# Kernel optimization log

Hardware: AMD Instinct MI355X
Metric: run time of the kernel (lower is better)

Reference implementation:

```python
import jax, jax.numpy as jnp
import numpy as np

B, S, D, H = 128, 256, 256, 8   # graphs, nodes/graph, dim_h, heads
N = B * S
E = 524288
DH = D // H
BN_EPS = 1e-5

def _bn(v, g, b):
    # BatchNorm1d forward with batch statistics (biased var), eval-dropout model
    m = v.mean(0)
    var = v.var(0)
    return (v - m) * jax.lax.rsqrt(var + BN_EPS) * g + b

def setup_inputs() -> dict:
    key = jax.random.key(0)
    ks = jax.random.split(key, 40)
    x = jax.random.normal(ks[0], (N, D), jnp.float32)
    src = jax.random.randint(ks[1], (E,), 0, N)
    dst = (src // S) * S + jax.random.randint(ks[2], (E,), 0, S)  # intra-graph edges
    edge_index = jnp.stack([src, dst]).astype(jnp.int64)
    def lin(k, i, o):
        return (jax.random.normal(k, (i, o), jnp.float32) / np.float32(np.sqrt(i)))
    inp = {
        'x': x, 'edge_index': edge_index,
        'W_gcn': lin(ks[3], D, D), 'b_gcn': jnp.zeros((D,), jnp.float32),
        'W_gin1': lin(ks[4], D, D), 'b_gin1': jnp.zeros((D,), jnp.float32),
        'W_gin2': lin(ks[5], D, D), 'b_gin2': jnp.zeros((D,), jnp.float32),
        'g_kv': jnp.ones((D,), jnp.float32), 'be_kv': jnp.zeros((D,), jnp.float32),
        'Wq1': lin(ks[6], D, D), 'bq1': jnp.zeros((D,), jnp.float32),
        'Wq2': lin(ks[7], D, D), 'bq2': jnp.zeros((D,), jnp.float32),
        'Wq_a': lin(ks[8], D, D), 'bq_a': jnp.zeros((D,), jnp.float32),
        'Wk_a': lin(ks[9], D, D), 'bk_a': jnp.zeros((D,), jnp.float32),
        'Wv_a': lin(ks[10], D, D), 'bv_a': jnp.zeros((D,), jnp.float32),
        'Wo_a': lin(ks[11], D, D), 'bo_a': jnp.zeros((D,), jnp.float32),
        'g_attn': jnp.ones((D,), jnp.float32), 'be_attn': jnp.zeros((D,), jnp.float32),
        'Wf1': lin(ks[12], D, 2 * D), 'bf1': jnp.zeros((2 * D,), jnp.float32),
        'Wf2': lin(ks[13], 2 * D, D), 'bf2': jnp.zeros((D,), jnp.float32),
        'g2': jnp.ones((D,), jnp.float32), 'be2': jnp.zeros((D,), jnp.float32),
    }
    return inp

def _forward(x, edge_index,
             W_gcn, b_gcn, W_gin1, b_gin1, W_gin2, b_gin2, g_kv, be_kv,
             Wq1, bq1, Wq2, bq2,
             Wq_a, bq_a, Wk_a, bk_a, Wv_a, bv_a, Wo_a, bo_a, g_attn, be_attn,
             Wf1, bf1, Wf2, bf2, g2, be2):
    row, col = edge_index[0], edge_index[1]
    h_in1 = x

    # ---- expert 0: GCNConv (add self loops + symmetric norm) ----
    loops = jnp.arange(N, dtype=row.dtype)
    row2 = jnp.concatenate([row, loops])
    col2 = jnp.concatenate([col, loops])
    deg = jax.ops.segment_sum(jnp.ones_like(row2, jnp.float32), col2, num_segments=N)
    dinv = jnp.where(deg > 0, jax.lax.rsqrt(deg), 0.0)
    norm = dinv[row2] * dinv[col2]                     # [E+N]
    xw = x @ W_gcn                                      # [N, D]
    h_gcn = jax.ops.segment_sum(norm[:, None] * xw[row2], col2, num_segments=N) + b_gcn
    e0 = _bn(h_gcn, g_kv, be_kv)

    # ---- expert 1: GINConv (eps=0, sum aggregation, 2-layer MLP) ----
    agg = jax.ops.segment_sum(x[row], col, num_segments=N)
    h_gin = jax.nn.relu((x + agg) @ W_gin1 + b_gin1) @ W_gin2 + b_gin2
    e1 = _bn(h_gin, g_kv, be_kv)

    # ---- global expert normalization (torch .std -> unbiased) ----
    allo = jnp.concatenate([e0, e1], axis=0)
    gm = allo.mean()
    gs = jnp.std(allo, ddof=1)
    e0 = (e0 - gm) / (gs + 1e-8)
    e1 = (e1 - gm) / (gs + 1e-8)

    # ---- uniform routing & kv residual mix ----
    kv = 0.5 * e0 + 0.5 * e1 + 0.1 * h_in1              # [N, D]

    # ---- dense batching (equal-sized graphs -> pure reshape, full mask) ----
    q_dense = h_in1.reshape(B, S, D)
    kv_dense = kv.reshape(B, S, D)

    # ---- q projection MLP ----
    q_dense = jax.nn.relu(q_dense @ Wq1 + bq1) @ Wq2 + bq2

    # ---- multihead attention (batch_first, no padding) ----
    qh = (q_dense @ Wq_a + bq_a).reshape(B, S, H, DH)
    kh = (kv_dense @ Wk_a + bk_a).reshape(B, S, H, DH)
    vh = (kv_dense @ Wv_a + bv_a).reshape(B, S, H, DH)
    scores = jnp.einsum('bqhd,bkhd->bhqk', qh, kh) / np.float32(np.sqrt(DH))
    attn = jax.nn.softmax(scores, axis=-1)
    o = jnp.einsum('bhqk,bkhd->bqhd', attn, vh).reshape(B, S, D)
    h_attn = (o @ Wo_a + bo_a).reshape(N, D)

    # ---- residual + norm + FFN block ----
    h = _bn(h_in1 + h_attn, g_attn, be_attn)
    h_ff = jax.nn.relu(h @ Wf1 + bf1) @ Wf2 + bf2
    h = _bn(h + h_ff, g2, be2)
    return h

def reference(x, edge_index,
              W_gcn, b_gcn, W_gin1, b_gin1, W_gin2, b_gin2, g_kv, be_kv,
              Wq1, bq1, Wq2, bq2,
              Wq_a, bq_a, Wk_a, bk_a, Wv_a, bv_a, Wo_a, bo_a, g_attn, be_attn,
              Wf1, bf1, Wf2, bf2, g2, be2):
    return _forward(x, edge_index,
                    W_gcn, b_gcn, W_gin1, b_gin1, W_gin2, b_gin2, g_kv, be_kv,
                    Wq1, bq1, Wq2, bq2,
                    Wq_a, bq_a, Wk_a, bk_a, Wv_a, bv_a, Wo_a, bo_a, g_attn, be_attn,
                    Wf1, bf1, Wf2, bf2, g2, be2)
```

## Files before the change

### kernel.cpp

```cpp
#include <hip/hip_runtime.h>
#include <hip/hip_bf16.h>

typedef __hip_bfloat16 bf16;
typedef __attribute__((ext_vector_type(8))) short short8;
typedef __attribute__((ext_vector_type(4))) short short4v;
typedef __attribute__((ext_vector_type(4))) float f32x4;
typedef __attribute__((ext_vector_type(4))) int i32x4;

#define N_ 32768
#define D_ 256
#define S_ 256
#define B_ 128
#define E_ 524288

static __device__ __forceinline__ f32x4 mfma16(short8 a, short8 b, f32x4 c) {
  return __builtin_amdgcn_mfma_f32_16x16x32_bf16(a, b, c, 0, 0, 0);
}
static __device__ __forceinline__ f32x4 fzero4() {
  f32x4 z; z[0] = 0.f; z[1] = 0.f; z[2] = 0.f; z[3] = 0.f; return z;
}
static __device__ __forceinline__ float bits2f(short s) {
  unsigned u = ((unsigned)(unsigned short)s) << 16;
  return __builtin_bit_cast(float, u);
}
static __device__ __forceinline__ short f2bits(float f) {
  bf16 b = __float2bfloat16(f);
  return __builtin_bit_cast(short, b);
}

#define GLOAD_LDS16(G, L) __builtin_amdgcn_global_load_lds( \
    (const __attribute__((address_space(1))) void*)(G),     \
    (__attribute__((address_space(3))) void*)(L), 16, 0, 0)

template<int F>
__global__ __launch_bounds__(256)
void gemm_bt(const bf16* __restrict__ A, const bf16* __restrict__ Bt,
             const float* __restrict__ bias, const float* __restrict__ biasB,
             const void* __restrict__ resid,
             float* __restrict__ Cf, bf16* __restrict__ Cb,
             float* __restrict__ Sp, float* __restrict__ SSp,
             int M, int Nc, int K, long bsA, long bsB, long bsC)
{
  __shared__ __align__(16) bf16 lA[128 * 32];
  __shared__ __align__(16) bf16 lB[128 * 32];
  __shared__ float sS[2][128], sSS[2][128];
  const int z = blockIdx.z;
  const bf16* Ab = A + (long)z * bsA;
  const bf16* Bb = Bt + (long)z * bsB;
  const int m0 = blockIdx.x * 128, n0 = blockIdx.y * 128;
  const int tid = threadIdx.x;
  const int lane = tid & 63;
  const int w = tid >> 6, wr = w >> 1, wc = w & 1;
  const int g = lane >> 4, r = lane & 15, ko = g * 8;
  const int srow = lane >> 2, skw = (lane & 3) * 8;

  f32x4 acc[4][4];
  for (int i = 0; i < 4; i++) for (int j = 0; j < 4; j++) acc[i][j] = fzero4();

  for (int k0 = 0; k0 < K; k0 += 32) {
    __syncthreads();
    for (int i = 0; i < 2; i++) {
      const int c = w * 2 + i;
      GLOAD_LDS16(Ab + (long)(m0 + c * 16 + srow) * K + k0 + skw, lA + c * 512);
      GLOAD_LDS16(Bb + (long)(n0 + c * 16 + srow) * K + k0 + skw, lB + c * 512);
    }
    __syncthreads();
    short8 af[4], bfv[4];
    for (int mi = 0; mi < 4; mi++)
      af[mi] = *(const short8*)&lA[(wr * 64 + mi * 16 + r) * 32 + ko];
    for (int ni = 0; ni < 4; ni++)
      bfv[ni] = *(const short8*)&lB[(wc * 64 + ni * 16 + r) * 32 + ko];
    for (int mi = 0; mi < 4; mi++)
      for (int ni = 0; ni < 4; ni++)
        acc[mi][ni] = mfma16(af[mi], bfv[ni], acc[mi][ni]);
  }

  float cs[4] = {0, 0, 0, 0}, css[4] = {0, 0, 0, 0};
  for (int mi = 0; mi < 4; mi++) for (int ni = 0; ni < 4; ni++) {
    const int row = m0 + wr * 64 + mi * 16 + g * 4;
    const int col = n0 + wc * 64 + ni * 16 + r;
    float bv = 0.0f;
    if (F & 2) {
      if ((F & 128) && col >= 256) bv = biasB[col - 256];
      else bv = bias[col];
    }
    for (int j = 0; j < 4; j++) {
      long idx = (long)(row + j) * Nc + col;
      float v = acc[mi][ni][j] + bv;
      if (F & 4)  v += ((const float*)resid)[(long)z * bsC + idx];
      if (F & 64) v += bits2f(((const short*)resid)[(long)z * bsC + idx]);
      if (F & 1)  v = fmaxf(v, 0.0f);
      if (F & 32) { cs[ni] += v; css[ni] += v * v; }
      if (F & 8)  Cf[(long)z * bsC + idx] = v;
      if (F & 16) Cb[(long)z * bsC + idx] = __float2bfloat16(v);
    }
  }
  if (F & 32) {
    for (int ni = 0; ni < 4; ni++) {
      cs[ni]  += __shfl_xor(cs[ni], 16);  cs[ni]  += __shfl_xor(cs[ni], 32);
      css[ni] += __shfl_xor(css[ni], 16); css[ni] += __shfl_xor(css[ni], 32);
    }
    if (lane < 16) {
      for (int ni = 0; ni < 4; ni++) {
        sS[wr][wc * 64 + ni * 16 + lane]  = cs[ni];
        sSS[wr][wc * 64 + ni * 16 + lane] = css[ni];
      }
    }
    __syncthreads();
    if (tid < 128) {
      atomicAdd(&Sp[n0 + tid],  sS[0][tid] + sS[1][tid]);
      atomicAdd(&SSp[n0 + tid], sSS[0][tid] + sSS[1][tid]);
    }
  }
}

template<int NS, int EP1, int EP2, bool STATS>
static __device__ __forceinline__ void mlp_body(
    const bf16* __restrict__ A, const bf16* __restrict__ B1,
    const bf16* __restrict__ B2, const bf16* __restrict__ B3,
    const float* __restrict__ bEp1, const float* __restrict__ bEp2,
    const float* __restrict__ bFin, const bf16* __restrict__ resid,
    bf16* __restrict__ out, float* __restrict__ Sp, float* __restrict__ SSp,
    bf16* lA, bf16* lB, bf16* lC)
{
  char* lCc = (char*)lC;
  const int tid = threadIdx.x;
  const int lane = tid & 63;
  const int w = tid >> 6;
  const int mh = w >> 2, nq = w & 3;
  const int g = lane >> 4, r = lane & 15, ko = g * 8;

  f32x4 acc[2][4];
  for (int i = 0; i < 2; i++) for (int j = 0; j < 4; j++) acc[i][j] = fzero4();

  for (int k0 = 0; k0 < 256; k0 += 32) {
    __syncthreads();
    if (tid < 256)
      GLOAD_LDS16(A + (long)(tid >> 2) * 256 + k0 + (tid & 3) * 8, lA + w * 512);
    GLOAD_LDS16(B1 + (long)(tid >> 2) * 256 + k0 + (tid & 3) * 8, lB + w * 512);
    GLOAD_LDS16(B1 + (long)((tid + 512) >> 2) * 256 + k0 + ((tid + 512) & 3) * 8,
                lB + w * 512 + 4096);
    __syncthreads();
    short8 af[2], bfv[4];
    for (int mi = 0; mi < 2; mi++)
      af[mi] = *(const short8*)&lA[(mh * 32 + mi * 16 + r) * 32 + ko];
    for (int ni = 0; ni < 4; ni++)
      bfv[ni] = *(const short8*)&lB[(nq * 64 + ni * 16 + r) * 32 + ko];
    for (int mi = 0; mi < 2; mi++)
      for (int ni = 0; ni < 4; ni++)
        acc[mi][ni] = mfma16(af[mi], bfv[ni], acc[mi][ni]);
  }
  for (int mi = 0; mi < 2; mi++) for (int ni = 0; ni < 4; ni++) {
    const int col = nq * 64 + ni * 16 + r;
    const float bv = (EP1 & 1) ? bEp1[col] : 0.0f;
    for (int j = 0; j < 4; j++) {
      const int row = mh * 32 + mi * 16 + g * 4 + j;
      float v = acc[mi][ni][j] + bv;
      if (EP1 & 4) v += bits2f(__builtin_bit_cast(short, resid[(long)row * 256 + col]));
      if (EP1 & 2) v = fmaxf(v, 0.0f);
      *(short*)(lCc + ((row * 512 + col * 2) ^ ((row & 7) << 4))) = f2bits(v);
    }
  }
  __syncthreads();

  for (int s = 2; s <= NS; s++) {
    const bf16* Bs = (s == 2) ? B2 : B3;
    for (int i = 0; i < 2; i++) for (int j = 0; j < 4; j++) acc[i][j] = fzero4();
    for (int k0 = 0; k0 < 256; k0 += 32) {
      __syncthreads();
      GLOAD_LDS16(Bs + (long)(tid >> 2) * 256 + k0 + (tid & 3) * 8, lB + w * 512);
      GLOAD_LDS16(Bs + (long)((tid + 512) >> 2) * 256 + k0 + ((tid + 512) & 3) * 8,
                  lB + w * 512 + 4096);
      __syncthreads();
      short8 af[2], bfv[4];
      for (int mi = 0; mi < 2; mi++) {
        const int row = mh * 32 + mi * 16 + r;
        af[mi] = *(const short8*)(lCc +
                  ((row * 512 + (k0 + ko) * 2) ^ ((row & 7) << 4)));
      }
      for (int ni = 0; ni < 4; ni++)
        bfv[ni] = *(const short8*)&lB[(nq * 64 + ni * 16 + r) * 32 + ko];
      for (int mi = 0; mi < 2; mi++)
        for (int ni = 0; ni < 4; ni++)
          acc[mi][ni] = mfma16(af[mi], bfv[ni], acc[mi][ni]);
    }
    if (s < NS) {
      __syncthreads();
      for (int mi = 0; mi < 2; mi++) for (int ni = 0; ni < 4; ni++) {
        const int col = nq * 64 + ni * 16 + r;
        const float bv = (EP2 & 1) ? bEp2[col] : 0.0f;
        for (int j = 0; j < 4; j++) {
          const int row = mh * 32 + mi * 16 + g * 4 + j;
          float v = acc[mi][ni][j] + bv;
          if (EP2 & 2) v = fmaxf(v, 0.0f);
          *(short*)(lCc + ((row * 512 + col * 2) ^ ((row & 7) << 4))) = f2bits(v);
        }
      }
      __syncthreads();
    }
  }

  float cs[4] = {0, 0, 0, 0}, css[4] = {0, 0, 0, 0};
  for (int mi = 0; mi < 2; mi++) for (int ni = 0; ni < 4; ni++) {
    const int col = nq * 64 + ni * 16 + r;
    const float bv = bFin[col];
    for (int j = 0; j < 4; j++) {
      const int row = mh * 32 + mi * 16 + g * 4 + j;
      float v = acc[mi][ni][j] + bv;
      if (STATS) { cs[ni] += v; css[ni] += v * v; }
      out[(long)row * 256 + col] = __float2bfloat16(v);
    }
  }
  if (STATS) {
    for (int ni = 0; ni < 4; ni++) {
      cs[ni]  += __shfl_xor(cs[ni], 16);  cs[ni]  += __shfl_xor(cs[ni], 32);
      css[ni] += __shfl_xor(css[ni], 16); css[ni] += __shfl_xor(css[ni], 32);
    }
    __syncthreads();
    float* sS = (float*)lC;
    if (lane < 16) {
      for (int ni = 0; ni < 4; ni++) {
        sS[mh * 256 + nq * 64 + ni * 16 + lane] = cs[ni];
        sS[512 + mh * 256 + nq * 64 + ni * 16 + lane] = css[ni];
      }
    }
    __syncthreads();
    if (tid < 256) {
      atomicAdd(&Sp[tid],  sS[tid] + sS[256 + tid]);
      atomicAdd(&SSp[tid], sS[512 + tid] + sS[768 + tid]);
    }
  }
}

__global__ __launch_bounds__(512)
void fused3_k(const bf16* __restrict__ adjGCNb, const bf16* __restrict__ adjGINb,
              const bf16* __restrict__ xT, const bf16* __restrict__ xb,
              const bf16* __restrict__ WgcnT, const bf16* __restrict__ Wgin1T,
              const bf16* __restrict__ Wgin2T, const bf16* __restrict__ Wq1T,
              const bf16* __restrict__ Wq2T, const bf16* __restrict__ WqaT,
              const float* __restrict__ b_gcn, const float* __restrict__ b_gin1,
              const float* __restrict__ b_gin2, const float* __restrict__ bq1,
              const float* __restrict__ bq2, const float* __restrict__ bq_a,
              bf16* __restrict__ hgcnb, bf16* __restrict__ hginb,
              bf16* __restrict__ qhb,
              float* __restrict__ S0, float* __restrict__ SS0,
              float* __restrict__ S1, float* __restrict__ SS1)
{
  __shared__ __align__(16) bf16 lA[64 * 32];
  __shared__ __align__(16) bf16 lB[256 * 32];
  __shared__ __align__(16) bf16 lC[64 * 256];
  const int bid = blockIdx.x;
  if (bid < 512) {
    const long g = bid >> 2;
    mlp_body<2, 0, 0, true>(adjGCNb + (long)bid * 16384, xT + g * 65536,
        WgcnT, nullptr, nullptr, nullptr, b_gcn, nullptr,
        hgcnb + (long)bid * 16384, S0, SS0, lA, lB, lC);
  } else if (bid < 1024) {
    const int sub = bid - 512;
    const long g = sub >> 2;
    mlp_body<3, 4, 3, true>(adjGINb + (long)sub * 16384, xT + g * 65536,
        Wgin1T, Wgin2T, nullptr, b_gin1, b_gin2, xb + (long)sub * 16384,
        hginb + (long)sub * 16384, S1, SS1, lA, lB, lC);
  } else {
    const int sub = bid - 1024;
    mlp_body<3, 3, 1, false>(xb + (long)sub * 16384, Wq1T, Wq2T, WqaT,
        bq1, bq2, bq_a, nullptr, qhb + (long)sub * 16384, nullptr, nullptr,
        lA, lB, lC);
  }
}

__global__ __launch_bounds__(256, 2)
void attn_k(const bf16* __restrict__ qh, const bf16* __restrict__ kh,
            const bf16* __restrict__ vh, bf16* __restrict__ ob, int ks)
{
  const int h = blockIdx.x, qhf = blockIdx.y, b = blockIdx.z;
  const int tid = threadIdx.x, lane = tid & 63, w = tid >> 6;
  const int g = lane >> 4, r = lane & 15, ko = g * 8;
  __shared__ __align__(16) bf16 lK[256 * 32];
  __shared__ __align__(16) bf16 lV[32 * 256];
  char* lKc = (char*)lK;
  char* lVc = (char*)lV;

  for (int i = 0; i < 4; i++) {
    int c = tid + i * 256;
    int row = c >> 2, p4 = c & 3;
    short8 v = *(const short8*)(kh + (long)(b * 256 + row) * ks + h * 32 + p4 * 8);
    *(short8*)(lKc + ((row * 64 + p4 * 16) ^ ((row & 7) << 4))) = v;
  }
  for (int i = 0; i < 2; i++) {
    int c = tid + i * 256;
    int sp = c >> 2, part = c & 3;
    const bf16* vp = vh + (long)(b * 256 + 2 * sp) * ks + h * 32 + part * 8;
    short8 va = *(const short8*)(vp);
    short8 vb = *(const short8*)(vp + ks);
    #pragma unroll
    for (int j = 0; j < 8; j++) {
      int dh = part * 8 + j;
      int sw = ((dh & 7) ^ ((dh >> 3) << 1)) & 7;
      unsigned wrd = ((unsigned)(unsigned short)vb[j] << 16) |
                     (unsigned)(unsigned short)va[j];
      *(unsigned*)(lVc + ((dh * 512 + sp * 4) ^ (sw << 4))) = wrd;
    }
  }
  __syncthreads();

  const float c1 = 0.17677669529663687f * 1.4426950408889634f;
  const int idx0 = (((lane >> 4) & 1) * 32 + r) * 4;
  const int idx1 = idx0 + 64;
  const bool selhi = lane >= 32;

  for (int mc = 0; mc < 2; mc++) {
    const long qbase = (long)b * 256 + qhf * 128 + w * 32 + mc * 16;
    short8 qf = *(const short8*)(qh + (qbase + r) * 256 + h * 32 + ko);
    f32x4 sc[16];
    __builtin_amdgcn_s_setprio(1);
    #pragma unroll
    for (int nc = 0; nc < 16; nc++) {
      int row = nc * 16 + r;
      short8 kf = *(const short8*)(lKc + ((row * 64 + g * 16) ^ ((r & 7) << 4)));
      sc[nc] = mfma16(kf, qf, fzero4());
    }
    __builtin_amdgcn_s_setprio(0);
    f32x4 m4 = sc[0];
    #pragma unroll
    for (int nc = 1; nc < 16; nc++)
      for (int j = 0; j < 4; j++) m4[j] = fmaxf(m4[j], sc[nc][j]);
    float mx = fmaxf(fmaxf(m4[0], m4[1]), fmaxf(m4[2], m4[3]));
    mx = fmaxf(mx, __shfl_xor(mx, 16));
    mx = fmaxf(mx, __shfl_xor(mx, 32));
    const float mxc = mx * c1;
    f32x4 s4 = fzero4();
    #pragma unroll
    for (int nc = 0; nc < 16; nc++)
      for (int j = 0; j < 4; j++) {
        float p = exp2f(fmaf(sc[nc][j], c1, -mxc));
        sc[nc][j] = p; s4[j] += p;
      }
    float sum = s4[0] + s4[1] + s4[2] + s4[3];
    sum += __shfl_xor(sum, 16);
    sum += __shfl_xor(sum, 32);
    const float invs = 1.0f / sum;
    f32x4 oa[2]; oa[0] = fzero4(); oa[1] = fzero4();
    __builtin_amdgcn_s_setprio(1);
    #pragma unroll
    for (int kc = 0; kc < 8; kc++) {
      int pkA0, pkA1, pkB0, pkB1;
      {
        const f32x4 pa = sc[2 * kc], pb = sc[2 * kc + 1];
        unsigned a0 = (unsigned short)f2bits(pa[0] * invs);
        unsigned a1 = (unsigned short)f2bits(pa[1] * invs);
        unsigned a2 = (unsigned short)f2bits(pa[2] * invs);
        unsigned a3 = (unsigned short)f2bits(pa[3] * invs);
        unsigned b0 = (unsigned short)f2bits(pb[0] * invs);
        unsigned b1 = (unsigned short)f2bits(pb[1] * invs);
        unsigned b2 = (unsigned short)f2bits(pb[2] * invs);
        unsigned b3 = (unsigned short)f2bits(pb[3] * invs);
        pkA0 = (int)((a1 << 16) | a0);
        pkA1 = (int)((a3 << 16) | a2);
        pkB0 = (int)((b1 << 16) | b0);
        pkB1 = (int)((b3 << 16) | b2);
      }
      int A0 = __builtin_amdgcn_ds_bpermute(idx0, pkA0);
      int A1 = __builtin_amdgcn_ds_bpermute(idx0, pkA1);
      int B0 = __builtin_amdgcn_ds_bpermute(idx0, pkB0);
      int B1 = __builtin_amdgcn_ds_bpermute(idx0, pkB1);
      int C0 = __builtin_amdgcn_ds_bpermute(idx1, pkA0);
      int C1 = __builtin_amdgcn_ds_bpermute(idx1, pkA1);
      int D0 = __builtin_amdgcn_ds_bpermute(idx1, pkB0);
      int D1 = __builtin_amdgcn_ds_bpermute(idx1, pkB1);
      i32x4 av;
      av[0] = selhi ? B0 : A0;
      av[1] = selhi ? B1 : A1;
      av[2] = selhi ? D0 : C0;
      av[3] = selhi ? D1 : C1;
      short8 af = __builtin_bit_cast(short8, av);
      #pragma unroll
      for (int n = 0; n < 2; n++) {
        int dh = n * 16 + r;
        int sw = ((dh & 7) ^ ((dh >> 3) << 1)) & 7;
        short8 bv = *(const short8*)(lVc + ((dh * 512 + kc * 64 + g * 16) ^ (sw << 4)));
        oa[n] = mfma16(af, bv, oa[n]);
      }
    }
    __builtin_amdgcn_s_setprio(0);
    #pragma unroll
    for (int n = 0; n < 2; n++)
      for (int j = 0; j < 4; j++)
        ob[(qbase + g * 4 + j) * 256 + h * 32 + n * 16 + r] =
          __float2bfloat16(oa[n][j]);
  }
}

__global__ __launch_bounds__(256)
void wprep_k(const float* w0, const float* w1, const float* w2, const float* w3,
             const float* w4, const float* w5, const float* w6, const float* w7,
             const float* w8, const float* wf1, const float* wf2,
             bf16* __restrict__ wT)
{
  __shared__ float tile[32][33];
  const float* srcs[9] = {w0, w1, w2, w3, w4, w5, w6, w7, w8};
  const int bid = blockIdx.x;
  const float* in; bf16* out; int in_rs, out_rs, bx, by;
  if (bid < 576) {
    int wi = bid >> 6, t = bid & 63;
    in = srcs[wi]; out = wT + (long)wi * 65536;
    in_rs = 256; out_rs = 256; bx = t & 7; by = t >> 3;
  } else if (bid < 704) {
    int t = bid - 576;
    in = wf1; out = wT + 589824;
    in_rs = 512; out_rs = 256; bx = t & 15; by = t >> 4;
  } else {
    int t = bid - 704;
    in = wf2; out = wT + 720896;
    in_rs = 256; out_rs = 512; bx = t & 7; by = t >> 3;
  }
  const int tx = threadIdx.x, ty = threadIdx.y;
  const int c = bx * 32 + tx;
  const int rb = by * 32;
  for (int i = 0; i < 4; i++)
    tile[ty + i * 8][tx] = in[(long)(rb + ty + i * 8) * in_rs + c];
  __syncthreads();
  const int oc = rb + tx;
  const int orb = bx * 32;
  for (int i = 0; i < 4; i++)
    out[(long)(orb + ty + i * 8) * out_rs + oc] =
      __float2bfloat16(tile[tx][ty + i * 8]);
}

__global__ __launch_bounds__(256)
void xprep_k(const float* __restrict__ x, bf16* __restrict__ xb,
             bf16* __restrict__ xT)
{
  __shared__ float tile[32][33];
  const int z = blockIdx.z;
  const long ioff = (long)z * 65536;
  const int tx = threadIdx.x, ty = threadIdx.y;
  const int c = blockIdx.x * 32 + tx;
  const int rb = blockIdx.y * 32;
  for (int i = 0; i < 4; i++) {
    float v = x[ioff + (long)(rb + ty + i * 8) * 256 + c];
    tile[ty + i * 8][tx] = v;
    xb[ioff + (long)(rb + ty + i * 8) * 256 + c] = __float2bfloat16(v);
  }
  __syncthreads();
  const int oc = rb + tx;
  const int orb = blockIdx.x * 32;
  for (int i = 0; i < 4; i++)
    xT[ioff + (long)(orb + ty + i * 8) * 256 + oc] =
      __float2bfloat16(tile[tx][ty + i * 8]);
}

__global__ __launch_bounds__(256)
void edge_cnt_k(const int* __restrict__ ei, unsigned* __restrict__ cnt)
{
  int e = blockIdx.x * 256 + threadIdx.x;
  int src = ei[e], dst = ei[E_ + e];
  long idx = ((long)(src >> 8) * 256 + (dst & 255)) * 256 + (src & 255);
  atomicAdd(&cnt[idx >> 2], 1u << ((idx & 3) * 8));
}

__global__ __launch_bounds__(256)
void deg_k(const unsigned* __restrict__ cnt, float* __restrict__ dinv)
{
  int rid = blockIdx.x * 16 + (threadIdx.x >> 4);
  int l16 = threadIdx.x & 15;
  uint4 v = ((const uint4*)(cnt + (long)rid * 64))[l16];
  unsigned s = 0;
  s += (v.x & 0xFF) + ((v.x >> 8) & 0xFF) + ((v.x >> 16) & 0xFF) + (v.x >> 24);
  s += (v.y & 0xFF) + ((v.y >> 8) & 0xFF) + ((v.y >> 16) & 0xFF) + (v.y >> 24);
  s += (v.z & 0xFF) + ((v.z >> 8) & 0xFF) + ((v.z >> 16) & 0xFF) + (v.z >> 24);
  s += (v.w & 0xFF) + ((v.w >> 8) & 0xFF) + ((v.w >> 16) & 0xFF) + (v.w >> 24);
  s += __shfl_xor(s, 1); s += __shfl_xor(s, 2);
  s += __shfl_xor(s, 4); s += __shfl_xor(s, 8);
  if (l16 == 0) dinv[rid] = rsqrtf((float)s + 1.0f);
}

__global__ __launch_bounds__(256)
void adj_derive_k(const unsigned* __restrict__ cnt, const float* __restrict__ dinv,
                  bf16* __restrict__ gin, bf16* __restrict__ gcn)
{
  long wi = (long)blockIdx.x * 256 + threadIdx.x;
  unsigned cw = cnt[wi];
  long i = wi * 4;
  float cv[4] = {(float)(cw & 0xFF), (float)((cw >> 8) & 0xFF),
                 (float)((cw >> 16) & 0xFF), (float)(cw >> 24)};
  long row = i >> 8;
  int g = (int)(row >> 8), dst = (int)(row & 255);
  int src0 = (int)(i & 255);
  float dd = dinv[row];
  const float* ds = dinv + (long)g * 256 + src0;
  short4v oi, oc;
  for (int j = 0; j < 4; j++) {
    float gv = cv[j] * dd * ds[j];
    if (src0 + j == dst) gv += dd * dd;
    oi[j] = f2bits(cv[j]);
    oc[j] = f2bits(gv);
  }
  *(short4v*)(gin + i) = oi;
  *(short4v*)(gcn + i) = oc;
}

__global__ __launch_bounds__(256)
void expert_stats_k(const float* __restrict__ S0, const float* __restrict__ SS0,
                    const float* __restrict__ S1, const float* __restrict__ SS1,
                    const float* __restrict__ gkv, const float* __restrict__ bkv,
                    float* __restrict__ kA, float* __restrict__ kB,
                    float* __restrict__ kC)
{
  const int d = threadIdx.x;
  const float invN = 1.0f / 32768.0f;
  float m0 = S0[d] * invN, v0 = SS0[d] * invN - m0 * m0;
  float a0 = gkv[d] * rsqrtf(v0 + 1e-5f), c0 = bkv[d] - m0 * a0;
  float m1 = S1[d] * invN, v1 = SS1[d] * invN - m1 * m1;
  float a1 = gkv[d] * rsqrtf(v1 + 1e-5f), c1 = bkv[d] - m1 * a1;
  float gsum = a0 * S0[d] + 32768.0f * c0 + a1 * S1[d] + 32768.0f * c1;
  float gss  = a0 * a0 * SS0[d] + 2.0f * a0 * c0 * S0[d] + 32768.0f * c0 * c0
             + a1 * a1 * SS1[d] + 2.0f * a1 * c1 * S1[d] + 32768.0f * c1 * c1;
  __shared__ float r1[256], r2[256];
  r1[d] = gsum; r2[d] = gss;
  __syncthreads();
  for (int s = 128; s > 0; s >>= 1) {
    if (d < s) { r1[d] += r1[d + s]; r2[d] += r2[d + s]; }
    __syncthreads();
  }
  const float cntall = 16777216.0f;
  float tg = r1[0], tss = r2[0];
  float gm = tg / cntall;
  float var = (tss - tg * tg / cntall) / (cntall - 1.0f);
  float gs = sqrtf(fmaxf(var, 0.f)) + 1e-8f;
  kA[d] = 0.5f * a0 / gs;
  kB[d] = 0.5f * a1 / gs;
  kC[d] = 0.5f * (c0 + c1 - 2.0f * gm) / gs;
}

__global__ __launch_bounds__(256)
void kv_mix_k(const bf16* __restrict__ hgcn, const bf16* __restrict__ hgin,
              const bf16* __restrict__ xb, const float* __restrict__ kA,
              const float* __restrict__ kB, const float* __restrict__ kC,
              bf16* __restrict__ kv)
{
  long i = ((long)blockIdx.x * 256 + threadIdx.x) * 8;
  int d0 = (int)(i & 255);
  short8 a = *(const short8*)(hgcn + i);
  short8 b = *(const short8*)(hgin + i);
  short8 c = *(const short8*)(xb + i);
  short8 o;
  for (int j = 0; j < 8; j++) {
    int d = d0 + j;
    float v = kA[d] * bits2f(a[j]) + kB[d] * bits2f(b[j]) + kC[d] + 0.1f * bits2f(c[j]);
    o[j] = f2bits(v);
  }
  *(short8*)(kv + i) = o;
}

template<int MODE>
__global__ __launch_bounds__(256)
void bn_apply_k(const bf16* __restrict__ in, const float* __restrict__ S,
                const float* __restrict__ SSq, const float* __restrict__ gg,
                const float* __restrict__ bb, float* __restrict__ outf,
                bf16* __restrict__ outb)
{
  long i = ((long)blockIdx.x * 256 + threadIdx.x) * 8;
  int d0 = (int)(i & 255);
  short8 v = *(const short8*)(in + i);
  const float invN = 1.0f / 32768.0f;
  float4 o0, o1; short8 o8;
  for (int j = 0; j < 8; j++) {
    int d = d0 + j;
    float m = S[d] * invN;
    float var = SSq[d] * invN - m * m;
    float a = gg[d] * rsqrtf(var + 1e-5f);
    float c = bb[d] - m * a;
    float o = a * bits2f(v[j]) + c;
    if (MODE & 1) { if (j < 4) (&o0.x)[j] = o; else (&o1.x)[j - 4] = o; }
    if (MODE & 2) o8[j] = f2bits(o);
  }
  if (MODE & 1) { *(float4*)(outf + i) = o0; *(float4*)(outf + i + 4) = o1; }
  if (MODE & 2) *(short8*)(outb + i) = o8;
}

static constexpr size_t OFF_S0 = 0, OFF_SS0 = 1024, OFF_S1 = 2048, OFF_SS1 = 3072;
static constexpr size_t OFF_S2 = 4096, OFF_SS2 = 5120, OFF_S3 = 6144, OFF_SS3 = 7168;
static constexpr size_t OFF_KA = 8192, OFF_KB = 9216, OFF_KC = 10240;
static constexpr size_t OFF_CNT = 16384;
static constexpr size_t CNT_BYTES = (size_t)B_ * S_ * S_;
static constexpr size_t ZERO_BYTES = OFF_CNT + CNT_BYTES;
static constexpr size_t OFF_DINV = OFF_CNT + (size_t)B_ * S_ * S_ * 2;
static constexpr size_t OFF_W = OFF_DINV + 131072;
static constexpr size_t NDB2 = (size_t)N_ * D_ * 2;
static constexpr size_t OFF_ADJGINB = OFF_W + 1703936;
static constexpr size_t OFF_ADJGCNB = OFF_ADJGINB + NDB2;
static constexpr size_t OFF_XB   = OFF_ADJGCNB + NDB2;
static constexpr size_t OFF_XT   = OFF_XB + NDB2;
static constexpr size_t OFF_AGG  = OFF_XT + NDB2;
static constexpr size_t OFF_GIN  = OFF_AGG + NDB2;
static constexpr size_t OFF_KV   = OFF_GIN + NDB2;
static constexpr size_t OFF_HGCN = OFF_KV + NDB2;
static constexpr size_t OFF_HGIN = OFF_HGCN + NDB2;

extern "C" void kernel_launch(void* const* d_in, const int* in_sizes, int n_in,
                              void* d_out, int out_size, void* d_ws, size_t ws_size,
                              hipStream_t stream)
{
  (void)in_sizes; (void)n_in; (void)out_size; (void)ws_size;
  const float* x      = (const float*)d_in[0];
  const int*   ei     = (const int*)d_in[1];
  const float* W_gcn  = (const float*)d_in[2];
  const float* b_gcn  = (const float*)d_in[3];
  const float* W_gin1 = (const float*)d_in[4];
  const float* b_gin1 = (const float*)d_in[5];
  const float* W_gin2 = (const float*)d_in[6];
  const float* b_gin2 = (const float*)d_in[7];
  const float* g_kv   = (const float*)d_in[8];
  const float* be_kv  = (const float*)d_in[9];
  const float* Wq1    = (const float*)d_in[10];
  const float* bq1    = (const float*)d_in[11];
  const float* Wq2    = (const float*)d_in[12];
  const float* bq2    = (const float*)d_in[13];
  const float* Wq_a   = (const float*)d_in[14];
  const float* bq_a   = (const float*)d_in[15];
  const float* Wk_a   = (const float*)d_in[16];
  const float* bk_a   = (const float*)d_in[17];
  const float* Wv_a   = (const float*)d_in[18];
  const float* bv_a   = (const float*)d_in[19];
  const float* Wo_a   = (const float*)d_in[20];
  const float* bo_a   = (const float*)d_in[21];
  const float* g_attn = (const float*)d_in[22];
  const float* be_attn= (const float*)d_in[23];
  const float* Wf1    = (const float*)d_in[24];
  const float* bf1    = (const float*)d_in[25];
  const float* Wf2    = (const float*)d_in[26];
  const float* bf2    = (const float*)d_in[27];
  const float* g2     = (const float*)d_in[28];
  const float* be2    = (const float*)d_in[29];

  char* ws = (char*)d_ws;
  float* S0  = (float*)(ws + OFF_S0);  float* SS0 = (float*)(ws + OFF_SS0);
  float* S1  = (float*)(ws + OFF_S1);  float* SS1 = (float*)(ws + OFF_SS1);
  float* S2  = (float*)(ws + OFF_S2);  float* SS2 = (float*)(ws + OFF_SS2);
  float* S3  = (float*)(ws + OFF_S3);  float* SS3 = (float*)(ws + OFF_SS3);
  float* kA  = (float*)(ws + OFF_KA);  float* kB  = (float*)(ws + OFF_KB);
  float* kC  = (float*)(ws + OFF_KC);
  unsigned* cntA = (unsigned*)(ws + OFF_CNT);
  float* dinv = (float*)(ws + OFF_DINV);
  bf16* wT = (bf16*)(ws + OFF_W);
  bf16 *WgcnT = wT,            *Wgin1T = wT + 65536,  *Wgin2T = wT + 131072;
  bf16 *Wq1T  = wT + 196608,   *Wq2T   = wT + 262144, *WqaT   = wT + 327680;
  bf16 *WkaT  = wT + 393216,   *WoaT   = wT + 524288;
  bf16 *Wf1T  = wT + 589824,   *Wf2T   = wT + 720896;
  bf16* adjGINb = (bf16*)(ws + OFF_ADJGINB);
  bf16* adjGCNb = (bf16*)(ws + OFF_ADJGCNB);
  bf16* xb    = (bf16*)(ws + OFF_XB);
  bf16* xT    = (bf16*)(ws + OFF_XT);
  bf16* kv_bf = (bf16*)(ws + OFF_KV);
  bf16* hgcnb = (bf16*)(ws + OFF_HGCN);
  bf16* hginb = (bf16*)(ws + OFF_HGIN);
  bf16* qhb    = (bf16*)(ws + OFF_CNT);
  bf16* khvb   = (bf16*)(ws + OFF_AGG);
  bf16* ob     = hginb;
  bf16* tbufb  = (bf16*)(ws + OFF_CNT);
  bf16* hb     = xb;
  bf16* f1b    = adjGINb;
  bf16* t2b    = (bf16*)(ws + OFF_CNT);
  float* outp  = (float*)d_out;

  hipMemsetAsync(d_ws, 0, ZERO_BYTES, stream);

  dim3 tb(32, 8);
  wprep_k<<<832, tb, 0, stream>>>(W_gcn, W_gin1, W_gin2, Wq1, Wq2,
                                  Wq_a, Wk_a, Wv_a, Wo_a, Wf1, Wf2, wT);
  xprep_k<<<dim3(8, 8, 128), tb, 0, stream>>>(x, xb, xT);
  edge_cnt_k<<<2048, 256, 0, stream>>>(ei, cntA);
  deg_k<<<2048, 256, 0, stream>>>(cntA, dinv);
  adj_derive_k<<<8192, 256, 0, stream>>>(cntA, dinv, adjGINb, adjGCNb);
  fused3_k<<<1536, 512, 0, stream>>>(adjGCNb, adjGINb, xT, xb,
      WgcnT, Wgin1T, Wgin2T, Wq1T, Wq2T, WqaT,
      b_gcn, b_gin1, b_gin2, bq1, bq2, bq_a,
      hgcnb, hginb, qhb, S0, SS0, S1, SS1);
  expert_stats_k<<<1, 256, 0, stream>>>(S0, SS0, S1, SS1, g_kv, be_kv, kA, kB, kC);
  kv_mix_k<<<4096, 256, 0, stream>>>(hgcnb, hginb, xb, kA, kB, kC, kv_bf);
  gemm_bt<146><<<dim3(256, 4, 1), 256, 0, stream>>>(kv_bf, WkaT, bk_a, bv_a,
      nullptr, nullptr, khvb, nullptr, nullptr, N_, 512, 256, 0, 0, 0);
  attn_k<<<dim3(8, 2, 128), 256, 0, stream>>>(qhb, khvb, khvb + 256, ob, 512);
  gemm_bt<114><<<dim3(256, 2, 1), 256, 0, stream>>>(ob, WoaT, bo_a, nullptr,
      xb, nullptr, tbufb, S2, SS2, N_, 256, 256, 0, 0, 0);
  bn_apply_k<2><<<4096, 256, 0, stream>>>(tbufb, S2, SS2, g_attn, be_attn, nullptr, hb);
  gemm_bt<19><<<dim3(256, 4, 1), 256, 0, stream>>>(hb, Wf1T, bf1, nullptr,
      nullptr, nullptr, f1b, nullptr, nullptr, N_, 512, 256, 0, 0, 0);
  gemm_bt<114><<<dim3(256, 2, 1), 256, 0, stream>>>(f1b, Wf2T, bf2, nullptr,
      hb, nullptr, t2b, S3, SS3, N_, 256, 512, 0, 0, 0);
  bn_apply_k<1><<<4096, 256, 0, stream>>>(t2b, S3, SS3, g2, be2, outp, nullptr);
}
```

Before: 320.7 us.

## Halve fused3 block to 256 threads with 64x64 per-wave MLP tiles

The chained-GEMM MLP body now runs with 4 waves per block instead of 8. Each wave covers all 64 rows and a 64-column slice, so its accumulator grows to 4x4 MFMA tiles and each A fragment read from LDS feeds more MFMAs. Each thread now issues four B-tile loads per k-step instead of two. The column-statistics reduction drops the LDS staging and two barriers in favour of direct per-wave atomics. The trade-off is higher register pressure, fewer waves to hide latency, and twice as many global atomics.

```diff
diff --git a/kernel.cpp b/kernel.cpp
--- a/kernel.cpp
+++ b/kernel.cpp
@@ -127,34 +127,35 @@
   const int tid = threadIdx.x;
   const int lane = tid & 63;
   const int w = tid >> 6;
-  const int mh = w >> 2, nq = w & 3;
   const int g = lane >> 4, r = lane & 15, ko = g * 8;
 
-  f32x4 acc[2][4];
-  for (int i = 0; i < 2; i++) for (int j = 0; j < 4; j++) acc[i][j] = fzero4();
+  f32x4 acc[4][4];
+  for (int i = 0; i < 4; i++) for (int j = 0; j < 4; j++) acc[i][j] = fzero4();
 
   for (int k0 = 0; k0 < 256; k0 += 32) {
     __syncthreads();
-    if (tid < 256)
-      GLOAD_LDS16(A + (long)(tid >> 2) * 256 + k0 + (tid & 3) * 8, lA + w * 512);
-    GLOAD_LDS16(B1 + (long)(tid >> 2) * 256 + k0 + (tid & 3) * 8, lB + w * 512);
-    GLOAD_LDS16(B1 + (long)((tid + 512) >> 2) * 256 + k0 + ((tid + 512) & 3) * 8,
-                lB + w * 512 + 4096);
+    GLOAD_LDS16(A + (long)(tid >> 2) * 256 + k0 + (tid & 3) * 8, lA + w * 512);
+    #pragma unroll
+    for (int i = 0; i < 4; i++) {
+      const int c = tid + i * 256;
+      GLOAD_LDS16(B1 + (long)(c >> 2) * 256 + k0 + (c & 3) * 8,
+                  lB + w * 512 + i * 2048);
+    }
     __syncthreads();
-    short8 af[2], bfv[4];
-    for (int mi = 0; mi < 2; mi++)
-      af[mi] = *(const short8*)&lA[(mh * 32 + mi * 16 + r) * 32 + ko];
+    short8 af[4], bfv[4];
+    for (int mi = 0; mi < 4; mi++)
+      af[mi] = *(const short8*)&lA[(mi * 16 + r) * 32 + ko];
     for (int ni = 0; ni < 4; ni++)
-      bfv[ni] = *(const short8*)&lB[(nq * 64 + ni * 16 + r) * 32 + ko];
-    for (int mi = 0; mi < 2; mi++)
+      bfv[ni] = *(const short8*)&lB[(w * 64 + ni * 16 + r) * 32 + ko];
+    for (int mi = 0; mi < 4; mi++)
       for (int ni = 0; ni < 4; ni++)
         acc[mi][ni] = mfma16(af[mi], bfv[ni], acc[mi][ni]);
   }
-  for (int mi = 0; mi < 2; mi++) for (int ni = 0; ni < 4; ni++) {
-    const int col = nq * 64 + ni * 16 + r;
+  for (int mi = 0; mi < 4; mi++) for (int ni = 0; ni < 4; ni++) {
+    const int col = w * 64 + ni * 16 + r;
     const float bv = (EP1 & 1) ? bEp1[col] : 0.0f;
     for (int j = 0; j < 4; j++) {
-      const int row = mh * 32 + mi * 16 + g * 4 + j;
+      const int row = mi * 16 + g * 4 + j;
       float v = acc[mi][ni][j] + bv;
       if (EP1 & 4) v += bits2f(__builtin_bit_cast(short, resid[(long)row * 256 + col]));
       if (EP1 & 2) v = fmaxf(v, 0.0f);
@@ -165,32 +166,35 @@
 
   for (int s = 2; s <= NS; s++) {
     const bf16* Bs = (s == 2) ? B2 : B3;
-    for (int i = 0; i < 2; i++) for (int j = 0; j < 4; j++) acc[i][j] = fzero4();
+    for (int i = 0; i < 4; i++) for (int j = 0; j < 4; j++) acc[i][j] = fzero4();
     for (int k0 = 0; k0 < 256; k0 += 32) {
       __syncthreads();
-      GLOAD_LDS16(Bs + (long)(tid >> 2) * 256 + k0 + (tid & 3) * 8, lB + w * 512);
-      GLOAD_LDS16(Bs + (long)((tid + 512) >> 2) * 256 + k0 + ((tid + 512) & 3) * 8,
-                  lB + w * 512 + 4096);
+      #pragma unroll
+      for (int i = 0; i < 4; i++) {
+        const int c = tid + i * 256;
+        GLOAD_LDS16(Bs + (long)(c >> 2) * 256 + k0 + (c & 3) * 8,
+                    lB + w * 512 + i * 2048);
+      }
       __syncthreads();
-      short8 af[2], bfv[4];
-      for (int mi = 0; mi < 2; mi++) {
-        const int row = mh * 32 + mi * 16 + r;
+      short8 af[4], bfv[4];
+      for (int mi = 0; mi < 4; mi++) {
+        const int row = mi * 16 + r;
         af[mi] = *(const short8*)(lCc +
                   ((row * 512 + (k0 + ko) * 2) ^ ((row & 7) << 4)));
       }
       for (int ni = 0; ni < 4; ni++)
-        bfv[ni] = *(const short8*)&lB[(nq * 64 + ni * 16 + r) * 32 + ko];
-      for (int mi = 0; mi < 2; mi++)
+        bfv[ni] = *(const short8*)&lB[(w * 64 + ni * 16 + r) * 32 + ko];
+      for (int mi = 0; mi < 4; mi++)
         for (int ni = 0; ni < 4; ni++)
           acc[mi][ni] = mfma16(af[mi], bfv[ni], acc[mi][ni]);
     }
     if (s < NS) {
       __syncthreads();
-      for (int mi = 0; mi < 2; mi++) for (int ni = 0; ni < 4; ni++) {
-        const int col = nq * 64 + ni * 16 + r;
+      for (int mi = 0; mi < 4; mi++) for (int ni = 0; ni < 4; ni++) {
+        const int col = w * 64 + ni * 16 + r;
         const float bv = (EP2 & 1) ? bEp2[col] : 0.0f;
         for (int j = 0; j < 4; j++) {
-          const int row = mh * 32 + mi * 16 + g * 4 + j;
+          const int row = mi * 16 + g * 4 + j;
           float v = acc[mi][ni][j] + bv;
           if (EP2 & 2) v = fmaxf(v, 0.0f);
           *(short*)(lCc + ((row * 512 + col * 2) ^ ((row & 7) << 4))) = f2bits(v);
@@ -201,11 +205,11 @@
   }
 
   float cs[4] = {0, 0, 0, 0}, css[4] = {0, 0, 0, 0};
-  for (int mi = 0; mi < 2; mi++) for (int ni = 0; ni < 4; ni++) {
-    const int col = nq * 64 + ni * 16 + r;
+  for (int mi = 0; mi < 4; mi++) for (int ni = 0; ni < 4; ni++) {
+    const int col = w * 64 + ni * 16 + r;
     const float bv = bFin[col];
     for (int j = 0; j < 4; j++) {
-      const int row = mh * 32 + mi * 16 + g * 4 + j;
+      const int row = mi * 16 + g * 4 + j;
       float v = acc[mi][ni][j] + bv;
       if (STATS) { cs[ni] += v; css[ni] += v * v; }
       out[(long)row * 256 + col] = __float2bfloat16(v);
@@ -216,23 +220,16 @@
       cs[ni]  += __shfl_xor(cs[ni], 16);  cs[ni]  += __shfl_xor(cs[ni], 32);
       css[ni] += __shfl_xor(css[ni], 16); css[ni] += __shfl_xor(css[ni], 32);
     }
-    __syncthreads();
-    float* sS = (float*)lC;
     if (lane < 16) {
       for (int ni = 0; ni < 4; ni++) {
-        sS[mh * 256 + nq * 64 + ni * 16 + lane] = cs[ni];
-        sS[512 + mh * 256 + nq * 64 + ni * 16 + lane] = css[ni];
-      }
-    }
-    __syncthreads();
-    if (tid < 256) {
-      atomicAdd(&Sp[tid],  sS[tid] + sS[256 + tid]);
-      atomicAdd(&SSp[tid], sS[512 + tid] + sS[768 + tid]);
-    }
-  }
-}
-
-__global__ __launch_bounds__(512)
+        atomicAdd(&Sp[w * 64 + ni * 16 + lane],  cs[ni]);
+        atomicAdd(&SSp[w * 64 + ni * 16 + lane], css[ni]);
+      }
+    }
+  }
+}
+
+__global__ __launch_bounds__(256)
 void fused3_k(const bf16* __restrict__ adjGCNb, const bf16* __restrict__ adjGINb,
               const bf16* __restrict__ xT, const bf16* __restrict__ xb,
               const bf16* __restrict__ WgcnT, const bf16* __restrict__ Wgin1T,
@@ -673,7 +670,7 @@
   edge_cnt_k<<<2048, 256, 0, stream>>>(ei, cntA);
   deg_k<<<2048, 256, 0, stream>>>(cntA, dinv);
   adj_derive_k<<<8192, 256, 0, stream>>>(cntA, dinv, adjGINb, adjGCNb);
-  fused3_k<<<1536, 512, 0, stream>>>(adjGCNb, adjGINb, xT, xb,
+  fused3_k<<<1536, 256, 0, stream>>>(adjGCNb, adjGINb, xT, xb,
       WgcnT, Wgin1T, Wgin2T, Wq1T, Wq2T, WqaT,
       b_gcn, b_gin1, b_gin2, bq1, bq2, bq_a,
       hgcnb, hginb, qhb, S0, SS0, S1, SS1);
```

After: 324.3 us. No clear change (+1.1%).

## Double-buffer LDS tiles in GEMM and fused MLP kernels to overlap loads

Applied to the files above, without the earlier changes.

Converts the K-loops of gemm_bt and mlp_body from single-buffered LDS staging (two barriers per step) to double buffering. The next K-slice is prefetched via global_load_lds into the alternate buffer while MFMAs run on the current one, with one barrier per step. LDS use doubles for lA and lB, which may lower occupancy. The barrier-count change also relies on the async LDS loads being complete at the single barrier (waitcnt), which the compiler must handle.

```diff
diff --git a/kernel.cpp b/kernel.cpp
--- a/kernel.cpp
+++ b/kernel.cpp
@@ -41,8 +41,8 @@
              float* __restrict__ Sp, float* __restrict__ SSp,
              int M, int Nc, int K, long bsA, long bsB, long bsC)
 {
-  __shared__ __align__(16) bf16 lA[128 * 32];
-  __shared__ __align__(16) bf16 lB[128 * 32];
+  __shared__ __align__(16) bf16 lA[2 * 128 * 32];
+  __shared__ __align__(16) bf16 lB[2 * 128 * 32];
   __shared__ float sS[2][128], sSS[2][128];
   const int z = blockIdx.z;
   const bf16* Ab = A + (long)z * bsA;
@@ -57,22 +57,33 @@
   f32x4 acc[4][4];
   for (int i = 0; i < 4; i++) for (int j = 0; j < 4; j++) acc[i][j] = fzero4();
 
+  for (int i = 0; i < 2; i++) {
+    const int c = w * 2 + i;
+    GLOAD_LDS16(Ab + (long)(m0 + c * 16 + srow) * K + skw, lA + c * 512);
+    GLOAD_LDS16(Bb + (long)(n0 + c * 16 + srow) * K + skw, lB + c * 512);
+  }
+  __syncthreads();
+
   for (int k0 = 0; k0 < K; k0 += 32) {
-    __syncthreads();
-    for (int i = 0; i < 2; i++) {
-      const int c = w * 2 + i;
-      GLOAD_LDS16(Ab + (long)(m0 + c * 16 + srow) * K + k0 + skw, lA + c * 512);
-      GLOAD_LDS16(Bb + (long)(n0 + c * 16 + srow) * K + k0 + skw, lB + c * 512);
-    }
-    __syncthreads();
+    const int cur = (k0 >> 5) & 1, nxt = cur ^ 1;
+    if (k0 + 32 < K) {
+      for (int i = 0; i < 2; i++) {
+        const int c = w * 2 + i;
+        GLOAD_LDS16(Ab + (long)(m0 + c * 16 + srow) * K + (k0 + 32) + skw,
+                    lA + nxt * 4096 + c * 512);
+        GLOAD_LDS16(Bb + (long)(n0 + c * 16 + srow) * K + (k0 + 32) + skw,
+                    lB + nxt * 4096 + c * 512);
+      }
+    }
     short8 af[4], bfv[4];
     for (int mi = 0; mi < 4; mi++)
-      af[mi] = *(const short8*)&lA[(wr * 64 + mi * 16 + r) * 32 + ko];
+      af[mi] = *(const short8*)&lA[cur * 4096 + (wr * 64 + mi * 16 + r) * 32 + ko];
     for (int ni = 0; ni < 4; ni++)
-      bfv[ni] = *(const short8*)&lB[(wc * 64 + ni * 16 + r) * 32 + ko];
+      bfv[ni] = *(const short8*)&lB[cur * 4096 + (wc * 64 + ni * 16 + r) * 32 + ko];
     for (int mi = 0; mi < 4; mi++)
       for (int ni = 0; ni < 4; ni++)
         acc[mi][ni] = mfma16(af[mi], bfv[ni], acc[mi][ni]);
+    __syncthreads();
   }
 
   float cs[4] = {0, 0, 0, 0}, css[4] = {0, 0, 0, 0};
@@ -133,22 +144,32 @@
   f32x4 acc[2][4];
   for (int i = 0; i < 2; i++) for (int j = 0; j < 4; j++) acc[i][j] = fzero4();
 
+  if (tid < 256)
+    GLOAD_LDS16(A + (long)(tid >> 2) * 256 + (tid & 3) * 8, lA + w * 512);
+  GLOAD_LDS16(B1 + (long)(tid >> 2) * 256 + (tid & 3) * 8, lB + w * 512);
+  GLOAD_LDS16(B1 + (long)((tid + 512) >> 2) * 256 + ((tid + 512) & 3) * 8,
+              lB + w * 512 + 4096);
+  __syncthreads();
   for (int k0 = 0; k0 < 256; k0 += 32) {
-    __syncthreads();
-    if (tid < 256)
-      GLOAD_LDS16(A + (long)(tid >> 2) * 256 + k0 + (tid & 3) * 8, lA + w * 512);
-    GLOAD_LDS16(B1 + (long)(tid >> 2) * 256 + k0 + (tid & 3) * 8, lB + w * 512);
-    GLOAD_LDS16(B1 + (long)((tid + 512) >> 2) * 256 + k0 + ((tid + 512) & 3) * 8,
-                lB + w * 512 + 4096);
-    __syncthreads();
+    const int cur = (k0 >> 5) & 1, nxt = cur ^ 1;
+    if (k0 + 32 < 256) {
+      if (tid < 256)
+        GLOAD_LDS16(A + (long)(tid >> 2) * 256 + (k0 + 32) + (tid & 3) * 8,
+                    lA + nxt * 2048 + w * 512);
+      GLOAD_LDS16(B1 + (long)(tid >> 2) * 256 + (k0 + 32) + (tid & 3) * 8,
+                  lB + nxt * 8192 + w * 512);
+      GLOAD_LDS16(B1 + (long)((tid + 512) >> 2) * 256 + (k0 + 32) + ((tid + 512) & 3) * 8,
+                  lB + nxt * 8192 + w * 512 + 4096);
+    }
     short8 af[2], bfv[4];
     for (int mi = 0; mi < 2; mi++)
-      af[mi] = *(const short8*)&lA[(mh * 32 + mi * 16 + r) * 32 + ko];
+      af[mi] = *(const short8*)&lA[cur * 2048 + (mh * 32 + mi * 16 + r) * 32 + ko];
     for (int ni = 0; ni < 4; ni++)
-      bfv[ni] = *(const short8*)&lB[(nq * 64 + ni * 16 + r) * 32 + ko];
+      bfv[ni] = *(const short8*)&lB[cur * 8192 + (nq * 64 + ni * 16 + r) * 32 + ko];
     for (int mi = 0; mi < 2; mi++)
       for (int ni = 0; ni < 4; ni++)
         acc[mi][ni] = mfma16(af[mi], bfv[ni], acc[mi][ni]);
+    __syncthreads();
   }
   for (int mi = 0; mi < 2; mi++) for (int ni = 0; ni < 4; ni++) {
     const int col = nq * 64 + ni * 16 + r;
@@ -166,12 +187,18 @@
   for (int s = 2; s <= NS; s++) {
     const bf16* Bs = (s == 2) ? B2 : B3;
     for (int i = 0; i < 2; i++) for (int j = 0; j < 4; j++) acc[i][j] = fzero4();
+    GLOAD_LDS16(Bs + (long)(tid >> 2) * 256 + (tid & 3) * 8, lB + w * 512);
+    GLOAD_LDS16(Bs + (long)((tid + 512) >> 2) * 256 + ((tid + 512) & 3) * 8,
+                lB + w * 512 + 4096);
+    __syncthreads();
     for (int k0 = 0; k0 < 256; k0 += 32) {
-      __syncthreads();
-      GLOAD_LDS16(Bs + (long)(tid >> 2) * 256 + k0 + (tid & 3) * 8, lB + w * 512);
-      GLOAD_LDS16(Bs + (long)((tid + 512) >> 2) * 256 + k0 + ((tid + 512) & 3) * 8,
-                  lB + w * 512 + 4096);
-      __syncthreads();
+      const int cur = (k0 >> 5) & 1, nxt = cur ^ 1;
+      if (k0 + 32 < 256) {
+        GLOAD_LDS16(Bs + (long)(tid >> 2) * 256 + (k0 + 32) + (tid & 3) * 8,
+                    lB + nxt * 8192 + w * 512);
+        GLOAD_LDS16(Bs + (long)((tid + 512) >> 2) * 256 + (k0 + 32) + ((tid + 512) & 3) * 8,
+                    lB + nxt * 8192 + w * 512 + 4096);
+      }
       short8 af[2], bfv[4];
       for (int mi = 0; mi < 2; mi++) {
         const int row = mh * 32 + mi * 16 + r;
@@ -179,13 +206,13 @@
                   ((row * 512 + (k0 + ko) * 2) ^ ((row & 7) << 4)));
       }
       for (int ni = 0; ni < 4; ni++)
-        bfv[ni] = *(const short8*)&lB[(nq * 64 + ni * 16 + r) * 32 + ko];
+        bfv[ni] = *(const short8*)&lB[cur * 8192 + (nq * 64 + ni * 16 + r) * 32 + ko];
       for (int mi = 0; mi < 2; mi++)
         for (int ni = 0; ni < 4; ni++)
           acc[mi][ni] = mfma16(af[mi], bfv[ni], acc[mi][ni]);
+      __syncthreads();
     }
     if (s < NS) {
-      __syncthreads();
       for (int mi = 0; mi < 2; mi++) for (int ni = 0; ni < 4; ni++) {
         const int col = nq * 64 + ni * 16 + r;
         const float bv = (EP2 & 1) ? bEp2[col] : 0.0f;
@@ -246,8 +273,8 @@
               float* __restrict__ S0, float* __restrict__ SS0,
               float* __restrict__ S1, float* __restrict__ SS1)
 {
-  __shared__ __align__(16) bf16 lA[64 * 32];
-  __shared__ __align__(16) bf16 lB[256 * 32];
+  __shared__ __align__(16) bf16 lA[2 * 64 * 32];
+  __shared__ __align__(16) bf16 lB[2 * 256 * 32];
   __shared__ __align__(16) bf16 lC[64 * 256];
   const int bid = blockIdx.x;
   if (bid < 512) {
```

Result: faster. 308.9 us (-3.7%).
